# Optimization experiments

Hardware: AMD Instinct MI355X
Metric: run time of the kernel (lower is better)

The kernel has to match this reference:

```python
import jax, jax.numpy as jnp
import numpy as np


def _reverse_sequence(x, lens):
    # TF-style reverse_sequence along axis 1: reverse the first lens[b] entries of row b.
    T = x.shape[1]
    t = jnp.arange(T)
    idx = jnp.where(t[None, :] < lens[:, None], lens[:, None] - 1 - t[None, :], t[None, :])
    idx = idx.reshape(idx.shape + (1,) * (x.ndim - 2))
    return jnp.take_along_axis(x, idx, axis=1)


def _crf_decode(potentials, transitions, seq_lens):
    # potentials: [B, T, O], transitions: [O, O], seq_lens: [B]
    B, T, O = potentials.shape
    init = potentials[:, 0, :]                                   # [B, O]
    valid = jnp.arange(1, T)[:, None] < seq_lens[None, :]        # [T-1, B]
    xs_pot = jnp.transpose(potentials[:, 1:, :], (1, 0, 2))      # [T-1, B, O]

    def fwd_step(state, xs):
        x_t, v = xs
        ts = state[:, :, None] + transitions[None, :, :]         # [B, prev, cur]
        new_state = jnp.where(v[:, None], x_t + jnp.max(ts, axis=1), state)
        bp = jnp.argmax(ts, axis=1).astype(jnp.int32)            # [B, O]
        sc = jnp.max(jax.nn.softmax(ts, axis=1), axis=1)         # [B, O] confidence of best transition
        return new_state, (bp, sc)

    last_score, (bps, scs) = jax.lax.scan(fwd_step, init, (xs_pot, valid))
    lens1 = jnp.maximum(seq_lens - 1, 0)
    bps = _reverse_sequence(jnp.transpose(bps, (1, 0, 2)), lens1)   # [B, T-1, O]
    scs = _reverse_sequence(jnp.transpose(scs, (1, 0, 2)), lens1)

    init_tag = jnp.argmax(last_score, axis=1).astype(jnp.int32)     # [B]
    init_conf = jnp.max(jax.nn.softmax(last_score, axis=1), axis=1) # [B]

    def bwd_step(tag, xs):
        bp_t, sc_t = xs
        new_tag = jnp.take_along_axis(bp_t, tag[:, None], axis=1)[:, 0]
        new_sc = jnp.take_along_axis(sc_t, tag[:, None], axis=1)[:, 0]
        return new_tag, (new_tag, new_sc)

    _, (tags, scores) = jax.lax.scan(
        bwd_step, init_tag,
        (jnp.transpose(bps, (1, 0, 2)), jnp.transpose(scs, (1, 0, 2))))
    decode_tags = _reverse_sequence(jnp.concatenate([init_tag[:, None], tags.T], axis=1), seq_lens)
    decode_scores = _reverse_sequence(jnp.concatenate([init_conf[:, None], scores.T], axis=1), seq_lens)
    return decode_tags, decode_scores


def setup_inputs() -> dict:
    key = jax.random.key(0)
    k1, k2, k3 = jax.random.split(key, 3)
    B, T, O = 512, 512, 64
    logits = jax.random.normal(k1, (B, T, O), dtype=jnp.float32)
    sequence_lengths = jax.random.randint(k2, (B,), 1, T + 1, dtype=jnp.int32)
    transition_params = jax.random.normal(k3, (O, O), dtype=jnp.float32) * 0.1
    return {"logits": logits, "transition_params": transition_params,
            "sequence_lengths": sequence_lengths}


def reference(logits, transition_params, sequence_lengths):
    pred_ids, scores = _crf_decode(logits, transition_params, sequence_lengths)
    T = pred_ids.shape[1]
    mask = jnp.arange(T)[None, :] < sequence_lengths[:, None]
    predicted_ids = pred_ids * mask.astype(pred_ids.dtype)
    confidence_values = scores * mask.astype(scores.dtype)
    return predicted_ids, confidence_values
```

## Files before the change

### kernel.cpp

```cpp
#include <hip/hip_runtime.h>
#include <math.h>

#define BB 512
#define TT 512
#define OO 64

__global__ __launch_bounds__(256) void crf_decode_kernel(
    const float* __restrict__ logits,
    const float* __restrict__ trans,
    const int*   __restrict__ seqlens,
    float* __restrict__ out)
{
    const int b   = blockIdx.x;
    const int tid = threadIdx.x;
    const int j   = tid >> 2;
    const int c   = tid & 3;

    __shared__ unsigned char bpl[TT][OO];
    __shared__ unsigned char scl[TT][OO];
    __shared__ float st[2][OO];

    const int L = seqlens[b];
    const float* lg = logits + (size_t)b * TT * OO;

    float trc[16];
    #pragma unroll
    for (int i2 = 0; i2 < 16; ++i2)
        trc[i2] = trans[(c * 16 + i2) * OO + j];

    if (tid < OO) st[0][tid] = lg[tid];
    __syncthreads();

    int cur = 0;
    for (int t = 1; t < L; ++t) {
        float x = lg[t * OO + j];

        float v[16];
        float m = -1e30f;
        int   idx = 0;
        #pragma unroll
        for (int i2 = 0; i2 < 16; ++i2) {
            float val = st[cur][c * 16 + i2] + trc[i2];
            v[i2] = val;
            if (val > m) { m = val; idx = c * 16 + i2; }
        }
        #pragma unroll
        for (int d = 1; d <= 2; d <<= 1) {
            float mo = __shfl_xor(m, d);
            int   io = __shfl_xor(idx, d);
            if (mo > m || (mo == m && io < idx)) { m = mo; idx = io; }
        }
        float s = 0.f;
        #pragma unroll
        for (int i2 = 0; i2 < 16; ++i2)
            s += __expf(v[i2] - m);
        #pragma unroll
        for (int d = 1; d <= 2; d <<= 1)
            s += __shfl_xor(s, d);

        if (c == 0) {
            st[cur ^ 1][j] = x + m;
            bpl[t][j] = (unsigned char)idx;
            float conf = 1.0f / s;
            conf = fminf(conf, 1.0f);
            scl[t][j] = (unsigned char)(conf * 255.0f + 0.5f);
        }
        cur ^= 1;
        __syncthreads();
    }

    if (tid == 0) {
        float m = -1e30f; int idx = 0;
        for (int jj = 0; jj < OO; ++jj) {
            float vv = st[cur][jj];
            if (vv > m) { m = vv; idx = jj; }
        }
        float s = 0.f;
        for (int jj = 0; jj < OO; ++jj)
            s += __expf(st[cur][jj] - m);

        float* out_tags   = out + (size_t)b * TT;
        float* out_scores = out + (size_t)BB * TT + (size_t)b * TT;
        out_tags[L - 1]   = (float)idx;
        out_scores[L - 1] = 1.0f / s;

        int tag = idx;
        for (int t = L - 1; t >= 1; --t) {
            int ntag  = bpl[t][tag];
            float sc  = (float)scl[t][tag] * (1.0f / 255.0f);
            out_tags[t - 1]   = (float)ntag;
            out_scores[t - 1] = sc;
            tag = ntag;
        }
    }

    float* out_tags   = out + (size_t)b * TT;
    float* out_scores = out + (size_t)BB * TT + (size_t)b * TT;
    for (int p = L + tid; p < TT; p += 256) {
        out_tags[p]   = 0.f;
        out_scores[p] = 0.f;
    }
}

extern "C" void kernel_launch(void* const* d_in, const int* in_sizes, int n_in,
                              void* d_out, int out_size, void* d_ws, size_t ws_size,
                              hipStream_t stream) {
    const float* logits = (const float*)d_in[0];
    const float* trans  = (const float*)d_in[1];
    const int*   lens   = (const int*)d_in[2];
    float* out = (float*)d_out;
    crf_decode_kernel<<<BB, 256, 0, stream>>>(logits, trans, lens, out);
}
```

Measured before the change: 413.0 us.

## Compute transition softmax via shared exp-factorization and spill confidences to workspace

The softmax denominator over previous states is factored as exp(state-mu)*exp(trans), so each step needs 64 exps in shared memory plus 16 FMAs per thread instead of 16 exps per thread. Confidence bytes now go to a global workspace instead of shared memory, which halves LDS use and should allow more blocks per CU (launch bounds 4). The next step's logit is prefetched, state is read with float4 loads, and the backtrace only records tags, with the scores gathered afterwards in parallel. In exchange it adds a second barrier per step and risks overflow or precision loss, because exp(state - state[0]) can grow large.

```diff
diff --git a/kernel.cpp b/kernel.cpp
--- a/kernel.cpp
+++ b/kernel.cpp
@@ -5,7 +5,130 @@
 #define TT 512
 #define OO 64
 
-__global__ __launch_bounds__(256) void crf_decode_kernel(
+__global__ __launch_bounds__(256, 4) void crf_fwd_kernel(
+    const float* __restrict__ logits,
+    const float* __restrict__ trans,
+    const int*   __restrict__ seqlens,
+    float* __restrict__ out,
+    unsigned char* __restrict__ confw)
+{
+    const int b   = blockIdx.x;
+    const int tid = threadIdx.x;
+    const int j   = tid >> 2;
+    const int c   = tid & 3;
+
+    __shared__ unsigned char bpl[TT][OO];
+    __shared__ float st[2][OO];
+    __shared__ float pl[OO];
+    __shared__ unsigned char tagl[TT];
+
+    const int L = seqlens[b];
+    const float* lg = logits + (size_t)b * TT * OO;
+    unsigned char* cw = confw + (size_t)b * TT * OO;
+
+    float trc[16], trcE[16];
+    #pragma unroll
+    for (int i2 = 0; i2 < 16; ++i2) {
+        float tv = trans[(c * 16 + i2) * OO + j];
+        trc[i2]  = tv;
+        trcE[i2] = __expf(tv);
+    }
+
+    if (tid < OO) st[0][tid] = lg[tid];
+    __syncthreads();
+
+    int cur = 0;
+    float xr = (c == 0 && L > 1) ? lg[OO + j] : 0.f;
+
+    for (int t = 1; t < L; ++t) {
+        float x = xr;
+        if (c == 0 && t + 1 < L) xr = lg[(t + 1) * OO + j];
+
+        const float4* stv = (const float4*)&st[cur][c * 16];
+        float4 s0 = stv[0], s1 = stv[1], s2 = stv[2], s3 = stv[3];
+        float v[16];
+        v[0]=s0.x+trc[0];  v[1]=s0.y+trc[1];  v[2]=s0.z+trc[2];  v[3]=s0.w+trc[3];
+        v[4]=s1.x+trc[4];  v[5]=s1.y+trc[5];  v[6]=s1.z+trc[6];  v[7]=s1.w+trc[7];
+        v[8]=s2.x+trc[8];  v[9]=s2.y+trc[9];  v[10]=s2.z+trc[10];v[11]=s2.w+trc[11];
+        v[12]=s3.x+trc[12];v[13]=s3.y+trc[13];v[14]=s3.z+trc[14];v[15]=s3.w+trc[15];
+
+        float m = -1e30f; int idx = 0;
+        #pragma unroll
+        for (int i2 = 0; i2 < 16; ++i2)
+            if (v[i2] > m) { m = v[i2]; idx = c * 16 + i2; }
+        #pragma unroll
+        for (int d = 1; d <= 2; d <<= 1) {
+            float mo = __shfl_xor(m, d);
+            int   io = __shfl_xor(idx, d);
+            if (mo > m || (mo == m && io < idx)) { m = mo; idx = io; }
+        }
+
+        float mu = st[cur][0];
+        if (tid < OO) pl[tid] = __expf(st[cur][tid] - mu);
+
+        if (c == 0) {
+            st[cur ^ 1][j] = x + m;
+            bpl[t][j] = (unsigned char)idx;
+        }
+        __syncthreads();
+
+        const float4* pv = (const float4*)&pl[c * 16];
+        float4 p0 = pv[0], p1 = pv[1], p2 = pv[2], p3 = pv[3];
+        float den =
+            p0.x*trcE[0]  + p0.y*trcE[1]  + p0.z*trcE[2]  + p0.w*trcE[3] +
+            p1.x*trcE[4]  + p1.y*trcE[5]  + p1.z*trcE[6]  + p1.w*trcE[7] +
+            p2.x*trcE[8]  + p2.y*trcE[9]  + p2.z*trcE[10] + p2.w*trcE[11] +
+            p3.x*trcE[12] + p3.y*trcE[13] + p3.z*trcE[14] + p3.w*trcE[15];
+        den += __shfl_xor(den, 1);
+        den += __shfl_xor(den, 2);
+
+        if (c == 0) {
+            float conf = __expf(m - mu) / den;
+            conf = fminf(conf, 1.0f);
+            cw[t * OO + j] = (unsigned char)(conf * 255.0f + 0.5f);
+        }
+        cur ^= 1;
+        __syncthreads();
+    }
+
+    if (tid == 0) {
+        float m = -1e30f; int idx = 0;
+        for (int jj = 0; jj < OO; ++jj) {
+            float vv = st[cur][jj];
+            if (vv > m) { m = vv; idx = jj; }
+        }
+        float s = 0.f;
+        for (int jj = 0; jj < OO; ++jj)
+            s += __expf(st[cur][jj] - m);
+
+        float* out_tags   = out + (size_t)b * TT;
+        float* out_scores = out + (size_t)BB * TT + (size_t)b * TT;
+        out_tags[L - 1]   = (float)idx;
+        out_scores[L - 1] = 1.0f / s;
+
+        int tag = idx;
+        tagl[L - 1] = (unsigned char)idx;
+        for (int t = L - 1; t >= 1; --t) {
+            tag = bpl[t][tag];
+            tagl[t - 1] = (unsigned char)tag;
+        }
+    }
+    __syncthreads();
+
+    float* out_tags   = out + (size_t)b * TT;
+    float* out_scores = out + (size_t)BB * TT + (size_t)b * TT;
+    for (int pos = tid; pos < L - 1; pos += 256) {
+        int tnext = pos + 1;
+        out_tags[pos]   = (float)tagl[pos];
+        out_scores[pos] = (float)cw[tnext * OO + tagl[tnext]] * (1.0f / 255.0f);
+    }
+    for (int pos = L + tid; pos < TT; pos += 256) {
+        out_tags[pos]   = 0.f;
+        out_scores[pos] = 0.f;
+    }
+}
+
+__global__ __launch_bounds__(256) void crf_decode_fallback(
     const float* __restrict__ logits,
     const float* __restrict__ trans,
     const int*   __restrict__ seqlens,
@@ -34,7 +157,6 @@
     int cur = 0;
     for (int t = 1; t < L; ++t) {
         float x = lg[t * OO + j];
-
         float v[16];
         float m = -1e30f;
         int   idx = 0;
@@ -109,5 +231,12 @@
     const float* trans  = (const float*)d_in[1];
     const int*   lens   = (const int*)d_in[2];
     float* out = (float*)d_out;
-    crf_decode_kernel<<<BB, 256, 0, stream>>>(logits, trans, lens, out);
+
+    const size_t need = (size_t)BB * TT * OO;
+    if (ws_size >= need) {
+        crf_fwd_kernel<<<BB, 256, 0, stream>>>(logits, trans, lens, out,
+                                               (unsigned char*)d_ws);
+    } else {
+        crf_decode_fallback<<<BB, 256, 0, stream>>>(logits, trans, lens, out);
+    }
 }
```

New measurement: 464.2 us. +12.4%, slower.

## Split CRF decode into a max-only scan and a parallel confidence pass

Applied to the files above, without the earlier changes.

The forward scan now uses one 64-thread wave per batch row, with one thread per output tag holding its full transition column in registers. It computes only max and argmax, and writes the per-step states to workspace memory. The softmax confidence is no longer computed for all tags at every step. A separate highly parallel kernel recomputes it only for the chosen tag path, using the stored states plus the transposed transition row. This removes exp work and block-wide barriers from the serial loop, at the cost of large workspace traffic and extra launches; when the workspace is too small, the old kernel runs as a fallback.

```diff
diff --git a/kernel.cpp b/kernel.cpp
--- a/kernel.cpp
+++ b/kernel.cpp
@@ -5,7 +5,130 @@
 #define TT 512
 #define OO 64
 
-__global__ __launch_bounds__(256) void crf_decode_kernel(
+__global__ void crf_transpose(const float* __restrict__ trans,
+                              float* __restrict__ Tt) {
+    for (int k = threadIdx.x; k < OO * OO; k += 256)
+        Tt[k] = trans[(k & 63) * OO + (k >> 6)];
+}
+
+__global__ __launch_bounds__(64) void crf_scan(
+    const float* __restrict__ logits,
+    const float* __restrict__ trans,
+    const int*   __restrict__ seqlens,
+    float* __restrict__ out_tags,
+    float* __restrict__ states)
+{
+    const int b = blockIdx.x;
+    const int j = threadIdx.x;
+
+    __shared__ __align__(16) float st[OO];
+    __shared__ unsigned char bpl[TT][OO];
+    __shared__ unsigned char tagl[TT];
+
+    const int L = seqlens[b];
+    const float* lg = logits + (size_t)b * TT * OO;
+    float* sout = states + (size_t)b * TT * OO;
+
+    float Tc[64];
+    #pragma unroll
+    for (int i = 0; i < 64; ++i)
+        Tc[i] = trans[i * OO + j];
+
+    float s = lg[j];
+    st[j] = s;
+    sout[j] = s;
+    asm volatile("" ::: "memory");
+
+    float xr = (L > 1) ? lg[OO + j] : 0.f;
+
+    for (int t = 1; t < L; ++t) {
+        float x = xr;
+        if (t + 1 < L) xr = lg[(t + 1) * OO + j];
+
+        float m = -1e30f; int idx = 0;
+        #pragma unroll
+        for (int g2 = 0; g2 < 16; ++g2) {
+            float4 sv = *(const float4*)&st[g2 * 4];
+            float c0 = sv.x + Tc[4*g2+0];
+            float c1 = sv.y + Tc[4*g2+1];
+            float c2 = sv.z + Tc[4*g2+2];
+            float c3 = sv.w + Tc[4*g2+3];
+            float m01 = fmaxf(c0, c1); int i01 = (c1 > c0) ? 4*g2+1 : 4*g2;
+            float m23 = fmaxf(c2, c3); int i23 = (c3 > c2) ? 4*g2+3 : 4*g2+2;
+            float mg  = fmaxf(m01, m23); int ig = (m23 > m01) ? i23 : i01;
+            if (g2 == 0) { m = mg; idx = ig; }
+            else { if (mg > m) idx = ig; m = fmaxf(m, mg); }
+        }
+
+        float snew = x + m;
+        bpl[t][j] = (unsigned char)idx;
+        sout[t * OO + j] = snew;
+        asm volatile("" ::: "memory");
+        st[j] = snew;
+        asm volatile("" ::: "memory");
+        s = snew;
+    }
+
+    float m = s; int idx = j;
+    #pragma unroll
+    for (int d = 1; d < 64; d <<= 1) {
+        float mo = __shfl_xor(m, d);
+        int   io = __shfl_xor(idx, d);
+        if (mo > m || (mo == m && io < idx)) { m = mo; idx = io; }
+    }
+
+    if (j == 0) {
+        int tag = idx;
+        tagl[L - 1] = (unsigned char)tag;
+        for (int t = L - 1; t >= 1; --t) {
+            tag = bpl[t][tag];
+            tagl[t - 1] = (unsigned char)tag;
+        }
+    }
+    asm volatile("" ::: "memory");
+
+    float* ot = out_tags + (size_t)b * TT;
+    for (int p = j; p < TT; p += 64)
+        ot[p] = (p < L) ? (float)tagl[p] : 0.f;
+}
+
+__global__ __launch_bounds__(256) void crf_conf(
+    const float* __restrict__ states,
+    const float* __restrict__ Tt,
+    const float* __restrict__ out_tags,
+    const int*   __restrict__ seqlens,
+    float* __restrict__ out_scores)
+{
+    const int b = blockIdx.x >> 7;
+    const int p = ((blockIdx.x & 127) << 2) + (threadIdx.x >> 6);
+    const int i = threadIdx.x & 63;
+    const int L = seqlens[b];
+
+    if (p >= L) {
+        if (i == 0) out_scores[(size_t)b * TT + p] = 0.f;
+        return;
+    }
+
+    float v = states[((size_t)b * TT + p) * OO + i];
+    if (p < L - 1) {
+        int g = (int)out_tags[(size_t)b * TT + p + 1];
+        v += Tt[g * OO + i];
+    }
+
+    float m = v;
+    #pragma unroll
+    for (int d = 1; d < 64; d <<= 1)
+        m = fmaxf(m, __shfl_xor(m, d));
+    float e = __expf(v - m);
+    #pragma unroll
+    for (int d = 1; d < 64; d <<= 1)
+        e += __shfl_xor(e, d);
+
+    if (i == 0)
+        out_scores[(size_t)b * TT + p] = 1.0f / e;
+}
+
+__global__ __launch_bounds__(256) void crf_decode_fallback(
     const float* __restrict__ logits,
     const float* __restrict__ trans,
     const int*   __restrict__ seqlens,
@@ -34,7 +157,6 @@
     int cur = 0;
     for (int t = 1; t < L; ++t) {
         float x = lg[t * OO + j];
-
         float v[16];
         float m = -1e30f;
         int   idx = 0;
@@ -50,19 +172,18 @@
             int   io = __shfl_xor(idx, d);
             if (mo > m || (mo == m && io < idx)) { m = mo; idx = io; }
         }
-        float s = 0.f;
+        float sden = 0.f;
         #pragma unroll
         for (int i2 = 0; i2 < 16; ++i2)
-            s += __expf(v[i2] - m);
+            sden += __expf(v[i2] - m);
         #pragma unroll
         for (int d = 1; d <= 2; d <<= 1)
-            s += __shfl_xor(s, d);
+            sden += __shfl_xor(sden, d);
 
         if (c == 0) {
             st[cur ^ 1][j] = x + m;
             bpl[t][j] = (unsigned char)idx;
-            float conf = 1.0f / s;
-            conf = fminf(conf, 1.0f);
+            float conf = fminf(1.0f / sden, 1.0f);
             scl[t][j] = (unsigned char)(conf * 255.0f + 0.5f);
         }
         cur ^= 1;
@@ -75,14 +196,14 @@
             float vv = st[cur][jj];
             if (vv > m) { m = vv; idx = jj; }
         }
-        float s = 0.f;
+        float sden = 0.f;
         for (int jj = 0; jj < OO; ++jj)
-            s += __expf(st[cur][jj] - m);
+            sden += __expf(st[cur][jj] - m);
 
         float* out_tags   = out + (size_t)b * TT;
         float* out_scores = out + (size_t)BB * TT + (size_t)b * TT;
         out_tags[L - 1]   = (float)idx;
-        out_scores[L - 1] = 1.0f / s;
+        out_scores[L - 1] = 1.0f / sden;
 
         int tag = idx;
         for (int t = L - 1; t >= 1; --t) {
@@ -109,5 +230,20 @@
     const float* trans  = (const float*)d_in[1];
     const int*   lens   = (const int*)d_in[2];
     float* out = (float*)d_out;
-    crf_decode_kernel<<<BB, 256, 0, stream>>>(logits, trans, lens, out);
-}
+
+    const size_t states_bytes = (size_t)BB * TT * OO * sizeof(float);
+    const size_t tt_bytes     = (size_t)OO * OO * sizeof(float);
+    if (ws_size >= states_bytes + tt_bytes) {
+        float* states = (float*)d_ws;
+        float* Tt     = (float*)((char*)d_ws + states_bytes);
+        float* out_tags   = out;
+        float* out_scores = out + (size_t)BB * TT;
+
+        crf_transpose<<<1, 256, 0, stream>>>(trans, Tt);
+        crf_scan<<<BB, 64, 0, stream>>>(logits, trans, lens, out_tags, states);
+        crf_conf<<<BB * 128, 256, 0, stream>>>(states, Tt, out_tags, lens,
+                                               out_scores);
+    } else {
+        crf_decode_fallback<<<BB, 256, 0, stream>>>(logits, trans, lens, out);
+    }
+}
```

Measured after the change: 474.3 us. 14.8% more time.
